# Kernel tuning notes

Measured on AMD Instinct MI355X. Metric: run time of the kernel, lower is better.

Reference implementation:

```python
import jax, jax.numpy as jnp
import numpy as np


def _bilinear_sample(img, gx, gy):
    """torch.nn.functional.grid_sample equivalent: bilinear, padding_mode='zeros',
    align_corners=True. img: [H,W]; gx,gy: normalized coords in [-1,1] (x->width, y->height)."""
    H, W = img.shape
    x = (gx + 1.0) * 0.5 * (W - 1)
    y = (gy + 1.0) * 0.5 * (H - 1)
    x0 = jnp.floor(x)
    y0 = jnp.floor(y)
    x1 = x0 + 1.0
    y1 = y0 + 1.0
    wx1 = x - x0
    wx0 = 1.0 - wx1
    wy1 = y - y0
    wy0 = 1.0 - wy1

    def gather(xi, yi):
        valid = (xi >= 0) & (xi <= W - 1) & (yi >= 0) & (yi <= H - 1)
        xc = jnp.clip(xi, 0, W - 1).astype(jnp.int32)
        yc = jnp.clip(yi, 0, H - 1).astype(jnp.int32)
        return jnp.where(valid, img[yc, xc], jnp.zeros((), img.dtype))

    return (gather(x0, y0) * wx0 * wy0 + gather(x1, y0) * wx1 * wy0 +
            gather(x0, y1) * wx0 * wy1 + gather(x1, y1) * wx1 * wy1)


def _radon_forward(img, n_angles, det_count, image_size, step_size, sampling_points):
    distance = 2.0 / image_size
    # detector shifts [D]
    sx = jnp.linspace(-1.0, 1.0, det_count) * (det_count / 2.0) * distance * step_size
    sy = -np.sqrt(2.0).astype(np.float32)
    ey = -sy
    angles = jnp.linspace(0.0, np.pi, n_angles)[:, None] + np.pi / 2.0  # [A,1]
    ca, sa = jnp.cos(angles), jnp.sin(angles)
    rsx = sx * ca - sy * sa            # [A,D] ray start x
    rsy = sx * sa + sy * ca            # [A,D] ray start y
    rdx = (sx * ca + sy * sa) - rsx    # rex - rsx  (ex=sx, ey=+sqrt2 => ex*ca - ey*sa)
    # careful: rex = ex*cos - ey*sin = sx*ca - ey*sa = sx*ca + sy*sa (since ey=-sy)
    rdy = (sx * sa - sy * ca) - rsy    # rey = ex*sin + ey*cos = sx*sa - sy*ca
    S = sampling_points
    t = (jnp.arange(S, dtype=jnp.float32) / S)[:, None, None]  # [S,1,1]
    gx = rsx[None] + t * rdx[None]     # [S,A,D]
    gy = rsy[None] + t * rdy[None]
    samples = _bilinear_sample(img, gx, gy)        # [S,A,D]
    intens = jnp.sum(samples, axis=0) / S          # [A,D]
    # torch.rot90(out, 2) on [A*D,1] then view(A,D) == flip both axes of [A,D]
    return jnp.flip(intens, (0, 1))


def setup_inputs() -> dict:
    key = jax.random.key(0)
    img = jax.random.uniform(key, (512, 512), dtype=jnp.float32)
    return {
        "input": img,
        "n_angles": 512,
        "det_count": 512,
        "image_size": 512,
        "step_size": 1,
        "sampling_points": 256,
    }


def reference(input, n_angles, det_count, image_size, step_size, sampling_points):
    return _radon_forward(input, n_angles, det_count, image_size, step_size, sampling_points)
```

## Files before the change

### kernel.cpp

```cpp
#include <hip/hip_runtime.h>
#include <math.h>
#include <stdint.h>

#define IMG 512
#define A_N 512
#define D_N 512
#define S_N 256
#define PAD 8
#define PW  528

typedef uint32_t Cell;

__device__ __forceinline__ uint32_t enc_e4m3_sw(float f) {
    union { float f; uint32_t u; } v; v.f = f;
    const uint32_t s = (v.u >> 24) & 0x80u;
    const int e = (int)((v.u >> 23) & 0xFFu);
    const uint32_t m = v.u & 0x7FFFFFu;
    if (e == 0) return s;
    int E = e - 120;
    if (E >= 16) return s | 0x7Eu;
    if (E >= 1) {
        uint32_t r = (m + (1u << 19)) >> 20;
        if (r >= 8u) { r = 0u; ++E; if (E >= 16) return s | 0x7Eu; }
        return s | ((uint32_t)E << 3) | r;
    }
    const int shift = 141 - e;
    if (shift > 24) return s;
    const uint32_t M = (1u << 23) | m;
    const uint32_t d = (M + (1u << (shift - 1))) >> shift;
    return (d >= 8u) ? (s | 0x08u) : (s | d);
}

__device__ __forceinline__ Cell cell_pack(float v00, float dx0,
                                          float v01, float dx1) {
#if __has_builtin(__builtin_amdgcn_cvt_pk_fp8_f32)
    int w = __builtin_amdgcn_cvt_pk_fp8_f32(v00, dx0, 0, false);
    w     = __builtin_amdgcn_cvt_pk_fp8_f32(v01, dx1, w, true);
    return (Cell)w;
#else
    return enc_e4m3_sw(v00) | (enc_e4m3_sw(dx0) << 8) |
           (enc_e4m3_sw(v01) << 16) | (enc_e4m3_sw(dx1) << 24);
#endif
}

__device__ __forceinline__ void cell_unpack(Cell w, float& v00, float& dx0,
                                            float& v01, float& dx1) {
#if __has_builtin(__builtin_amdgcn_cvt_pk_f32_fp8)
    typedef float f2v __attribute__((ext_vector_type(2)));
    const f2v lo = __builtin_amdgcn_cvt_pk_f32_fp8((int)w, false);
    const f2v hi = __builtin_amdgcn_cvt_pk_f32_fp8((int)w, true);
    v00 = lo.x; dx0 = lo.y; v01 = hi.x; dx1 = hi.y;
#else
    auto dec = [](uint32_t b) -> float {
        const uint32_t s = b >> 7, e = (b >> 3) & 15u, m = b & 7u;
        float v = e ? ldexpf((float)(8u + m), (int)e - 10)
                    : ldexpf((float)m, -9);
        return s ? -v : v;
    };
    v00 = dec(w & 255u); dx0 = dec((w >> 8) & 255u);
    v01 = dec((w >> 16) & 255u); dx1 = dec(w >> 24);
#endif
}

__device__ __forceinline__ float imz(const float* __restrict__ im, int y, int x) {
    return ((unsigned)y < 512u && (unsigned)x < 512u) ? im[(y << 9) + x] : 0.0f;
}

__global__ __launch_bounds__(256)
void pack_fp8(const float* __restrict__ im,
              Cell* __restrict__ pack, Cell* __restrict__ packT) {
    __shared__ Cell ldsT[32][33];
    const int bx = blockIdx.x % 17, by = blockIdx.x / 17;
    const int tx = threadIdx.x & 31, ty0 = threadIdx.x >> 5;
    const int p = bx * 32 + tx;
    const int x = p - PAD;
    #pragma unroll
    for (int i = 0; i < 4; ++i) {
        const int ty = ty0 + i * 8;
        const int q = by * 32 + ty;
        const int y = q - PAD;
        const float a = imz(im, y, x);
        const float b = imz(im, y, x + 1);
        const float c = imz(im, y + 1, x);
        const float d = imz(im, y + 1, x + 1);
        if (p < PW && q < PW)
            pack[q * PW + p] = cell_pack(a, b - a, c, d - c);
        ldsT[tx][ty] = cell_pack(a, c - a, b, d - b);
    }
    __syncthreads();
    #pragma unroll
    for (int i = 0; i < 4; ++i) {
        const int r  = ty0 + i * 8;
        const int qT = bx * 32 + r;
        const int pT = by * 32 + tx;
        if (qT < PW && pT < PW)
            packT[qT * PW + pT] = ldsT[r][tx];
    }
}

struct Samp { Cell w; float fx, fy; };

__device__ __forceinline__ Samp samp_load(const Cell* __restrict__ base,
                                          float Ax, float Ay,
                                          float dBx, float dBy, int s) {
    Samp r;
    const float x = fmaf((float)s, dBx, Ax);
    const float y = fmaf((float)s, dBy, Ay);
    const int ix = (int)x, iy = (int)y;
    r.w  = base[iy * PW + ix];
    r.fx = x - (float)ix;
    r.fy = y - (float)iy;
    return r;
}

__device__ __forceinline__ void samp_acc(const Samp& r, float& acc) {
    float v00, dx0, v01, dx1;
    cell_unpack(r.w, v00, dx0, v01, dx1);
    const float t_ = fmaf(r.fx, dx0, v00);
    const float b_ = fmaf(r.fx, dx1, v01);
    acc = fmaf(r.fy, b_ - t_, t_ + acc);
}

__global__ __launch_bounds__(256, 8)
void radon_fp8(const Cell* __restrict__ pack, const Cell* __restrict__ packT,
               float* __restrict__ out) {
    const int blk  = blockIdx.x;
    const int a    = ((blk & 7) << 6) | ((blk >> 3) & 63);
    const int dg   = (int)((0x70615243u >> ((blk >> 9) * 4)) & 7u);
    const int w    = threadIdx.x >> 6;
    const int lane = threadIdx.x & 63;
    const int di   = lane & 15;
    const int js   = lane >> 4;
    const int d    = dg * 64 + w * 16 + di;

    const float PI  = 3.14159265358979323846f;
    const float SQ2 = 1.41421356237309504880f;

    const float ang = fmaf((float)a, PI / 511.0f, PI * 0.5f);
    float sa, ca;
    sincosf(ang, &sa, &ca);

    const float sx = fmaf((float)d, 2.0f / 511.0f, -1.0f);
    float Ax = (fmaf(sx, ca,  SQ2 * sa) + 1.0f) * 255.5f;
    float Ay = (fmaf(sx, sa, -SQ2 * ca) + 1.0f) * 255.5f;
    float Bx = -2.0f * SQ2 * sa * 255.5f;
    float By =  2.0f * SQ2 * ca * 255.5f;

    const Cell* base = pack;
    if (fabsf(sa) > fabsf(ca)) {
        float t;
        t = Ax; Ax = Ay; Ay = t;
        t = Bx; Bx = By; By = t;
        base = packT;
    }

    float t0 = 0.0f, t1 = 255.0f / 256.0f;
    bool ok = true;
    {
        const float ra = (-1.0f - Ax) / Bx, rb = (512.0f - Ax) / Bx;
        t0 = fmaxf(t0, fminf(ra, rb));
        t1 = fminf(t1, fmaxf(ra, rb));
    }
    if (fabsf(By) > 1e-9f) {
        const float ra = (-1.0f - Ay) / By, rb = (512.0f - Ay) / By;
        t0 = fmaxf(t0, fminf(ra, rb));
        t1 = fminf(t1, fmaxf(ra, rb));
    } else if (Ay < -1.0f || Ay > 512.0f) ok = false;

    float acc0 = 0.0f, acc1 = 0.0f, acc2 = 0.0f, acc3 = 0.0f;
    if (ok && t0 <= t1) {
        const int s0  = max(0, (int)(t0 * 256.0f) - 1);
        const int s1  = min(S_N - 1, (int)(t1 * 256.0f) + 1);
        const int m   = s1 - (s0 + js);
        const int nk  = (m >= 0) ? ((m >> 2) + 1) : 0;

        const float dBx = Bx * (1.0f / 256.0f);
        const float dBy = By * (1.0f / 256.0f);
        Ax += (float)PAD;
        Ay += (float)PAD;

        int s = s0 + js;
        int k = 0;
        const int nFull = nk >> 2;
        if (nFull > 0) {
            Samp c0 = samp_load(base, Ax, Ay, dBx, dBy, s);
            Samp c1 = samp_load(base, Ax, Ay, dBx, dBy, s + 4);
            Samp c2 = samp_load(base, Ax, Ay, dBx, dBy, s + 8);
            Samp c3 = samp_load(base, Ax, Ay, dBx, dBy, s + 12);
            for (int g = 1; g < nFull; ++g) {
                Samp n0 = samp_load(base, Ax, Ay, dBx, dBy, s + 16);
                Samp n1 = samp_load(base, Ax, Ay, dBx, dBy, s + 20);
                Samp n2 = samp_load(base, Ax, Ay, dBx, dBy, s + 24);
                Samp n3 = samp_load(base, Ax, Ay, dBx, dBy, s + 28);
                samp_acc(c0, acc0);
                samp_acc(c1, acc1);
                samp_acc(c2, acc2);
                samp_acc(c3, acc3);
                c0 = n0; c1 = n1; c2 = n2; c3 = n3;
                s += 16;
            }
            samp_acc(c0, acc0);
            samp_acc(c1, acc1);
            samp_acc(c2, acc2);
            samp_acc(c3, acc3);
            s += 16;
            k = nFull << 2;
        }
        for (; k < nk; ++k, s += 4) {
            Samp r = samp_load(base, Ax, Ay, dBx, dBy, s);
            samp_acc(r, acc0);
        }
    }
    float acc = (acc0 + acc1) + (acc2 + acc3);

    acc += __shfl_xor(acc, 16);
    acc += __shfl_xor(acc, 32);

    __shared__ float red[64];
    if (lane < 16) red[w * 16 + di] = acc;
    __syncthreads();
    if (threadIdx.x < 64) {
        const float v = red[threadIdx.x] * (1.0f / 256.0f);
        const int dd = dg * 64 + threadIdx.x;
        out[(511 - a) * 512 + (511 - dd)] = v;
    }
}

__global__ __launch_bounds__(256)
void radon_direct(const float* __restrict__ img, float* __restrict__ out) {
    const int tid = blockIdx.x * 256 + threadIdx.x;
    const int d = tid & (D_N - 1);
    const int a = tid >> 9;
    const float PI  = 3.14159265358979323846f;
    const float SQ2 = 1.41421356237309504880f;
    const float ang = fmaf((float)a, PI / 511.0f, PI * 0.5f);
    float sa, ca;
    sincosf(ang, &sa, &ca);
    const float sx = fmaf((float)d, 2.0f / 511.0f, -1.0f);
    const float Ax = (fmaf(sx, ca,  SQ2 * sa) + 1.0f) * 255.5f;
    const float Ay = (fmaf(sx, sa, -SQ2 * ca) + 1.0f) * 255.5f;
    const float Bx = -2.0f * SQ2 * sa * 255.5f;
    const float By =  2.0f * SQ2 * ca * 255.5f;
    float acc = 0.0f;
    for (int s = 0; s < S_N; ++s) {
        const float t = (float)s * (1.0f / 256.0f);
        const float x = fmaf(t, Bx, Ax);
        const float y = fmaf(t, By, Ay);
        const float xf = floorf(x), yf = floorf(y);
        const float fx = x - xf, fy = y - yf;
        const int ix = (int)xf, iy = (int)yf;
        float wx0 = 1.0f - fx, wx1 = fx, wy0 = 1.0f - fy, wy1 = fy;
        wx0 = ((unsigned)ix       < 512u) ? wx0 : 0.0f;
        wx1 = ((unsigned)(ix + 1) < 512u) ? wx1 : 0.0f;
        wy0 = ((unsigned)iy       < 512u) ? wy0 : 0.0f;
        wy1 = ((unsigned)(iy + 1) < 512u) ? wy1 : 0.0f;
        const int ix0 = min(max(ix, 0), 511), ix1 = min(max(ix + 1, 0), 511);
        const int iy0 = min(max(iy, 0), 511), iy1 = min(max(iy + 1, 0), 511);
        const float* r0 = img + (iy0 << 9);
        const float* r1 = img + (iy1 << 9);
        acc = fmaf(fmaf(r0[ix1], wx1, r0[ix0] * wx0), wy0, acc);
        acc = fmaf(fmaf(r1[ix1], wx1, r1[ix0] * wx0), wy1, acc);
    }
    out[(511 - a) * 512 + (511 - d)] = acc * (1.0f / 256.0f);
}

extern "C" void kernel_launch(void* const* d_in, const int* in_sizes, int n_in,
                              void* d_out, int out_size, void* d_ws, size_t ws_size,
                              hipStream_t stream) {
    const float* img = (const float*)d_in[0];
    float* out = (float*)d_out;
    const size_t packBytes = (size_t)PW * PW * sizeof(Cell);

    if (ws_size >= 2 * packBytes) {
        Cell* pack  = (Cell*)d_ws;
        Cell* packT = pack + (size_t)PW * PW;
        pack_fp8<<<17 * 17, 256, 0, stream>>>(img, pack, packT);
        radon_fp8<<<4096, 256, 0, stream>>>(pack, packT, out);
    } else {
        radon_direct<<<(A_N * D_N) / 256, 256, 0, stream>>>(img, out);
    }
}
```

Baseline: 111.1 us.

## Process two mirrored detector groups per block and use hardware fract

Each block now handles two detector groups (j and 7-j) in sequence, pairing long central rays with short edge rays to balance the work per block. The grid is halved to 2048 blocks. Per-angle setup (sincos, reciprocals of Bx/By) is hoisted and shared across both groups, and the ray-clip divides become multiplies. The fractional sample weights now come from the amdgcn fract builtin. The trade-off is fewer blocks in flight and two serial passes per block.

```diff
diff --git a/kernel.cpp b/kernel.cpp
--- a/kernel.cpp
+++ b/kernel.cpp
@@ -59,6 +59,14 @@
     };
     v00 = dec(w & 255u); dx0 = dec((w >> 8) & 255u);
     v01 = dec((w >> 16) & 255u); dx1 = dec(w >> 24);
+#endif
+}
+
+__device__ __forceinline__ float fract_fast(float x) {
+#if __has_builtin(__builtin_amdgcn_fractf)
+    return __builtin_amdgcn_fractf(x);
+#else
+    return x - floorf(x);
 #endif
 }
 
@@ -108,8 +116,8 @@
     const float y = fmaf((float)s, dBy, Ay);
     const int ix = (int)x, iy = (int)y;
     r.w  = base[iy * PW + ix];
-    r.fx = x - (float)ix;
-    r.fy = y - (float)iy;
+    r.fx = fract_fast(x);
+    r.fy = fract_fast(y);
     return r;
 }
 
@@ -126,12 +134,11 @@
                float* __restrict__ out) {
     const int blk  = blockIdx.x;
     const int a    = ((blk & 7) << 6) | ((blk >> 3) & 63);
-    const int dg   = (int)((0x70615243u >> ((blk >> 9) * 4)) & 7u);
+    const int j    = blk >> 9;
     const int w    = threadIdx.x >> 6;
     const int lane = threadIdx.x & 63;
     const int di   = lane & 15;
     const int js   = lane >> 4;
-    const int d    = dg * 64 + w * 16 + di;
 
     const float PI  = 3.14159265358979323846f;
     const float SQ2 = 1.41421356237309504880f;
@@ -140,89 +147,96 @@
     float sa, ca;
     sincosf(ang, &sa, &ca);
 
-    const float sx = fmaf((float)d, 2.0f / 511.0f, -1.0f);
-    float Ax = (fmaf(sx, ca,  SQ2 * sa) + 1.0f) * 255.5f;
-    float Ay = (fmaf(sx, sa, -SQ2 * ca) + 1.0f) * 255.5f;
+    float ux = ca, uy = sa;
+    float cx = fmaf(fmaf(SQ2, sa, 1.0f), 255.5f, (float)PAD);
+    float cy = fmaf(fmaf(-SQ2, ca, 1.0f), 255.5f, (float)PAD);
     float Bx = -2.0f * SQ2 * sa * 255.5f;
     float By =  2.0f * SQ2 * ca * 255.5f;
 
     const Cell* base = pack;
     if (fabsf(sa) > fabsf(ca)) {
         float t;
-        t = Ax; Ax = Ay; Ay = t;
+        t = ux; ux = uy; uy = t;
+        t = cx; cx = cy; cy = t;
         t = Bx; Bx = By; By = t;
         base = packT;
     }
-
-    float t0 = 0.0f, t1 = 255.0f / 256.0f;
-    bool ok = true;
-    {
-        const float ra = (-1.0f - Ax) / Bx, rb = (512.0f - Ax) / Bx;
+    const float rBx = 1.0f / Bx, rBy = 1.0f / By;
+    const float dBx = Bx * (1.0f / 256.0f);
+    const float dBy = By * (1.0f / 256.0f);
+    const float XLO = (float)PAD - 1.0f;
+    const float XHI = (float)PAD + 512.0f;
+
+    __shared__ float red[2][64];
+
+    #pragma unroll 1
+    for (int pi = 0; pi < 2; ++pi) {
+        const int dg = pi ? (7 - j) : j;
+        const int dd = dg * 64 + w * 16 + di;
+        const float df = (float)dd - 255.5f;
+        const float Ax = fmaf(df, ux, cx);
+        const float Ay = fmaf(df, uy, cy);
+
+        float ra = (XLO - Ax) * rBx, rb = (XHI - Ax) * rBx;
+        float t0 = fmaxf(0.0f, fminf(ra, rb));
+        float t1 = fminf(255.0f / 256.0f, fmaxf(ra, rb));
+        ra = (XLO - Ay) * rBy; rb = (XHI - Ay) * rBy;
         t0 = fmaxf(t0, fminf(ra, rb));
         t1 = fminf(t1, fmaxf(ra, rb));
-    }
-    if (fabsf(By) > 1e-9f) {
-        const float ra = (-1.0f - Ay) / By, rb = (512.0f - Ay) / By;
-        t0 = fmaxf(t0, fminf(ra, rb));
-        t1 = fminf(t1, fmaxf(ra, rb));
-    } else if (Ay < -1.0f || Ay > 512.0f) ok = false;
-
-    float acc0 = 0.0f, acc1 = 0.0f, acc2 = 0.0f, acc3 = 0.0f;
-    if (ok && t0 <= t1) {
-        const int s0  = max(0, (int)(t0 * 256.0f) - 1);
-        const int s1  = min(S_N - 1, (int)(t1 * 256.0f) + 1);
-        const int m   = s1 - (s0 + js);
-        const int nk  = (m >= 0) ? ((m >> 2) + 1) : 0;
-
-        const float dBx = Bx * (1.0f / 256.0f);
-        const float dBy = By * (1.0f / 256.0f);
-        Ax += (float)PAD;
-        Ay += (float)PAD;
-
-        int s = s0 + js;
-        int k = 0;
-        const int nFull = nk >> 2;
-        if (nFull > 0) {
-            Samp c0 = samp_load(base, Ax, Ay, dBx, dBy, s);
-            Samp c1 = samp_load(base, Ax, Ay, dBx, dBy, s + 4);
-            Samp c2 = samp_load(base, Ax, Ay, dBx, dBy, s + 8);
-            Samp c3 = samp_load(base, Ax, Ay, dBx, dBy, s + 12);
-            for (int g = 1; g < nFull; ++g) {
-                Samp n0 = samp_load(base, Ax, Ay, dBx, dBy, s + 16);
-                Samp n1 = samp_load(base, Ax, Ay, dBx, dBy, s + 20);
-                Samp n2 = samp_load(base, Ax, Ay, dBx, dBy, s + 24);
-                Samp n3 = samp_load(base, Ax, Ay, dBx, dBy, s + 28);
+
+        float acc0 = 0.0f, acc1 = 0.0f, acc2 = 0.0f, acc3 = 0.0f;
+        if (t0 <= t1) {
+            const int s0  = max(0, (int)(t0 * 256.0f) - 1);
+            const int s1  = min(S_N - 1, (int)(t1 * 256.0f) + 1);
+            const int m   = s1 - (s0 + js);
+            const int nk  = (m >= 0) ? ((m >> 2) + 1) : 0;
+
+            int s = s0 + js;
+            int k = 0;
+            const int nFull = nk >> 2;
+            if (nFull > 0) {
+                Samp c0 = samp_load(base, Ax, Ay, dBx, dBy, s);
+                Samp c1 = samp_load(base, Ax, Ay, dBx, dBy, s + 4);
+                Samp c2 = samp_load(base, Ax, Ay, dBx, dBy, s + 8);
+                Samp c3 = samp_load(base, Ax, Ay, dBx, dBy, s + 12);
+                for (int g = 1; g < nFull; ++g) {
+                    Samp n0 = samp_load(base, Ax, Ay, dBx, dBy, s + 16);
+                    Samp n1 = samp_load(base, Ax, Ay, dBx, dBy, s + 20);
+                    Samp n2 = samp_load(base, Ax, Ay, dBx, dBy, s + 24);
+                    Samp n3 = samp_load(base, Ax, Ay, dBx, dBy, s + 28);
+                    samp_acc(c0, acc0);
+                    samp_acc(c1, acc1);
+                    samp_acc(c2, acc2);
+                    samp_acc(c3, acc3);
+                    c0 = n0; c1 = n1; c2 = n2; c3 = n3;
+                    s += 16;
+                }
                 samp_acc(c0, acc0);
                 samp_acc(c1, acc1);
                 samp_acc(c2, acc2);
                 samp_acc(c3, acc3);
-                c0 = n0; c1 = n1; c2 = n2; c3 = n3;
                 s += 16;
+                k = nFull << 2;
             }
-            samp_acc(c0, acc0);
-            samp_acc(c1, acc1);
-            samp_acc(c2, acc2);
-            samp_acc(c3, acc3);
-            s += 16;
-            k = nFull << 2;
+            for (; k < nk; ++k, s += 4) {
+                Samp r = samp_load(base, Ax, Ay, dBx, dBy, s);
+                samp_acc(r, acc0);
+            }
         }
-        for (; k < nk; ++k, s += 4) {
-            Samp r = samp_load(base, Ax, Ay, dBx, dBy, s);
-            samp_acc(r, acc0);
-        }
-    }
-    float acc = (acc0 + acc1) + (acc2 + acc3);
-
-    acc += __shfl_xor(acc, 16);
-    acc += __shfl_xor(acc, 32);
-
-    __shared__ float red[64];
-    if (lane < 16) red[w * 16 + di] = acc;
+        float acc = (acc0 + acc1) + (acc2 + acc3);
+
+        acc += __shfl_xor(acc, 16);
+        acc += __shfl_xor(acc, 32);
+        if (lane < 16) red[pi][w * 16 + di] = acc;
+    }
+
     __syncthreads();
-    if (threadIdx.x < 64) {
-        const float v = red[threadIdx.x] * (1.0f / 256.0f);
-        const int dd = dg * 64 + threadIdx.x;
-        out[(511 - a) * 512 + (511 - dd)] = v;
+    if (threadIdx.x < 128) {
+        const int pi2 = threadIdx.x >> 6;
+        const int t   = threadIdx.x & 63;
+        const int dg  = pi2 ? (7 - j) : j;
+        const int dd  = dg * 64 + t;
+        out[(511 - a) * 512 + (511 - dd)] = red[pi2][t] * (1.0f / 256.0f);
     }
 }
 
@@ -275,7 +289,7 @@
         Cell* pack  = (Cell*)d_ws;
         Cell* packT = pack + (size_t)PW * PW;
         pack_fp8<<<17 * 17, 256, 0, stream>>>(img, pack, packT);
-        radon_fp8<<<4096, 256, 0, stream>>>(pack, packT, out);
+        radon_fp8<<<2048, 256, 0, stream>>>(pack, packT, out);
     } else {
         radon_direct<<<(A_N * D_N) / 256, 256, 0, stream>>>(img, out);
     }
```

Result: no change. 111.0 us (-0.0%).
